# Kernel tuning notes

Measured on AMD Instinct MI355X. Metric: run time of the kernel, lower is better.

Reference implementation:

```python
import jax, jax.numpy as jnp
import numpy as np

B, S, IN, OUT = 2, 2048, 4096, 4096


def setup_inputs() -> dict:
    key = jax.random.key(0)
    k1, k2, k3, k4, k5 = jax.random.split(key, 5)
    x = jax.random.normal(k1, (B, S, IN), dtype=jnp.float32)
    weight_int8 = jax.random.randint(k2, (OUT, IN), 0, 127, dtype=jnp.int32)
    weight_scales = jax.random.uniform(k3, (OUT,), dtype=jnp.float32)
    weight_fp = jax.random.normal(k4, (OUT, IN), dtype=jnp.float32) * 0.02
    bias = jax.random.normal(k5, (OUT,), dtype=jnp.float32) * 0.02
    return {"x": x, "weight_int8": weight_int8, "weight_scales": weight_scales,
            "weight_fp": weight_fp, "bias": bias}


def reference(x, weight_int8, weight_scales, weight_fp, bias):
    # Dequantize: per-row scale / 127, cast to activation dtype (matches
    # torch: weight_int8.to(dtype) * (scales.unsqueeze(1)/127).to(dtype)).
    w_dq = weight_int8.astype(x.dtype) * (weight_scales[:, None] / 127.0).astype(x.dtype)
    # out = x @ w_dq.T + bias, over flattened leading dims
    out = jnp.einsum('bsi,oi->bso', x, w_dq) + bias
    return out
```

## Files before the change

kernel.cpp:

```cpp
#include <hip/hip_runtime.h>
#include <hip/hip_bf16.h>
#include <stdint.h>

#define MDIM 4096
#define NDIM 4096
#define KDIM 4096
#define NT   (KDIM / 64)

typedef __attribute__((ext_vector_type(4))) float  f32x4;
typedef __attribute__((ext_vector_type(4))) int    i32x4;
typedef __attribute__((ext_vector_type(8))) short  bf16x8;
typedef __attribute__((ext_vector_type(4))) float  fx4;
typedef __attribute__((ext_vector_type(4))) int    ix4;
typedef __attribute__((ext_vector_type(8))) unsigned short usx8;

__device__ static inline unsigned short f32_to_bf16_rne(float f) {
  union { float f; unsigned int u; } v; v.f = f;
  unsigned int u = v.u;
  u += 0x7fffu + ((u >> 16) & 1u);
  return (unsigned short)(u >> 16);
}

__device__ static inline void gload_lds16(const void* g, void* l) {
  __builtin_amdgcn_global_load_lds((const __attribute__((address_space(1))) void*)g,
                                   (__attribute__((address_space(3))) void*)l,
                                   16, 0, 0);
}

__device__ static inline void mfma_i8(i32x4& d, const i32x4& a, const i32x4& b) {
  asm("v_mfma_i32_16x16x64_i8 %0, %1, %2, %0" : "+v"(d) : "v"(a), "v"(b));
}


__global__ __launch_bounds__(256) void quant_both(
    const float* __restrict__ x, const int* __restrict__ w8,
    signed char* __restrict__ xq, signed char* __restrict__ wq,
    float* __restrict__ xs) {
  const int bid = blockIdx.x, t = threadIdx.x;
  if (bid < MDIM) {
    const float* row = x + (size_t)bid * KDIM + t * 16;
    fx4 v0 = *(const fx4*)(row);
    fx4 v1 = *(const fx4*)(row + 4);
    fx4 v2 = *(const fx4*)(row + 8);
    fx4 v3 = *(const fx4*)(row + 12);
    float am = 0.0f;
#pragma unroll
    for (int j = 0; j < 4; ++j) {
      am = fmaxf(am, fmaxf(__builtin_fabsf(v0[j]), __builtin_fabsf(v1[j])));
      am = fmaxf(am, fmaxf(__builtin_fabsf(v2[j]), __builtin_fabsf(v3[j])));
    }
#pragma unroll
    for (int off = 32; off; off >>= 1) am = fmaxf(am, __shfl_xor(am, off));
    __shared__ float wm[4];
    if ((t & 63) == 0) wm[t >> 6] = am;
    __syncthreads();
    am = fmaxf(fmaxf(wm[0], wm[1]), fmaxf(wm[2], wm[3]));
    am = fmaxf(am, 1e-20f);
    const float qs = 127.0f / am;
    int q[16];
#pragma unroll
    for (int j = 0; j < 4; ++j) {
      q[j]      = (int)rintf(v0[j] * qs);
      q[4 + j]  = (int)rintf(v1[j] * qs);
      q[8 + j]  = (int)rintf(v2[j] * qs);
      q[12 + j] = (int)rintf(v3[j] * qs);
    }
    i32x4 pk;
#pragma unroll
    for (int j = 0; j < 4; ++j)
      pk[j] = (q[4*j] & 255) | ((q[4*j+1] & 255) << 8) |
              ((q[4*j+2] & 255) << 16) | ((q[4*j+3] & 255) << 24);
    *(i32x4*)(xq + (size_t)bid * KDIM + t * 16) = pk;
    if (t == 0) xs[bid] = am * (1.0f / 127.0f);
  } else {
    const int n = bid - MDIM;
    const int* row = w8 + (size_t)n * KDIM + t * 16;
    ix4 w0 = *(const ix4*)(row);
    ix4 w1 = *(const ix4*)(row + 4);
    ix4 w2 = *(const ix4*)(row + 8);
    ix4 w3 = *(const ix4*)(row + 12);
    i32x4 pk;
    pk[0] = (w0[0] & 255) | ((w0[1] & 255) << 8) | ((w0[2] & 255) << 16) | ((w0[3] & 255) << 24);
    pk[1] = (w1[0] & 255) | ((w1[1] & 255) << 8) | ((w1[2] & 255) << 16) | ((w1[3] & 255) << 24);
    pk[2] = (w2[0] & 255) | ((w2[1] & 255) << 8) | ((w2[2] & 255) << 16) | ((w2[3] & 255) << 24);
    pk[3] = (w3[0] & 255) | ((w3[1] & 255) << 8) | ((w3[2] & 255) << 16) | ((w3[3] & 255) << 24);
    *(i32x4*)(wq + (size_t)n * KDIM + t * 16) = pk;
  }
}


__global__ __launch_bounds__(256, 4) void gemm_i8(
    const signed char* __restrict__ Aq,
    const signed char* __restrict__ Wq,
    const float* __restrict__ xs,
    const float* __restrict__ scales,
    const float* __restrict__ bias,
    float* __restrict__ C) {
  __shared__ signed char Ash[2 * 8192];
  __shared__ signed char Bsh[2 * 8192];

  const int tid = threadIdx.x;
  const int w   = tid >> 6;
  const int l   = tid & 63;
  const int wr  = w >> 1;
  const int wc  = w & 1;
  const int fr  = l & 15;
  const int fq  = l >> 4;

  const int id  = blockIdx.x;
  const int swz = (id & 7) * 128 + (id >> 3);
  const int bm  = swz >> 5, bn = swz & 31;

  const signed char* aorg = Aq + (size_t)(bm * 128) * KDIM;
  const signed char* borg = Wq + (size_t)(bn * 128) * KDIM;

  const int ks = (l & 3) ^ ((l >> 3) & 3);
  const size_t g_off = (size_t)(w * 16 + (l >> 2)) * KDIM + (size_t)ks * 16;
  const int    s_off = w * 1024;

#define STAGE(isB, t, P, h) do {                                                \
    const signed char* _g = ((isB) ? borg : aorg)                               \
        + (size_t)(h) * 64 * KDIM + (size_t)(t) * 64 + g_off;                   \
    signed char* _l = ((isB) ? Bsh : Ash) + ((P) + (h) * 4096 + s_off);         \
    gload_lds16(_g, _l);                                                        \
  } while (0)

  const int sl    = (fq ^ ((fr >> 1) & 3)) * 16;
  const int abase = (wr * 64 + fr) * 64 + sl;
  const int bbase = (wc * 64 + fr) * 64 + sl;

#define BAR   __builtin_amdgcn_s_barrier()
#define LGKM0 asm volatile("s_waitcnt lgkmcnt(0)" ::: "memory")
#define VM0   asm volatile("s_waitcnt vmcnt(0)" ::: "memory")

  i32x4 acc[4][4] = {};
  i32x4 a[4], b[4];

  STAGE(0, 0, 0, 0); STAGE(0, 0, 0, 1); STAGE(1, 0, 0, 0); STAGE(1, 0, 0, 1);
  VM0;
  BAR;

#pragma unroll 2
  for (int u = 0; u < NT; ++u) {
    const int cp = (u & 1) * 8192;
    const int np = cp ^ 8192;
    if (u + 1 < NT) {
      STAGE(0, u + 1, np, 0); STAGE(0, u + 1, np, 1);
      STAGE(1, u + 1, np, 0); STAGE(1, u + 1, np, 1);
    }
#pragma unroll
    for (int rb = 0; rb < 4; ++rb) a[rb] = *(const i32x4*)(Ash + cp + abase + rb * 1024);
#pragma unroll
    for (int cb = 0; cb < 4; ++cb) b[cb] = *(const i32x4*)(Bsh + cp + bbase + cb * 1024);
#pragma unroll
    for (int rb = 0; rb < 4; ++rb)
#pragma unroll
      for (int cb = 0; cb < 4; ++cb)
        mfma_i8(acc[rb][cb], a[rb], b[cb]);
    LGKM0;
    VM0;
    BAR;
  }

#undef STAGE

  const float inv127 = 1.0f / 127.0f;
  const int m_base = bm * 128 + wr * 64 + fq * 4;
  const int n_base = bn * 128 + wc * 64;
  float xr[4][4];
#pragma unroll
  for (int rb = 0; rb < 4; ++rb)
#pragma unroll
    for (int r = 0; r < 4; ++r) xr[rb][r] = xs[m_base + rb * 16 + r];
#pragma unroll
  for (int cb = 0; cb < 4; ++cb) {
    const int n = n_base + cb * 16 + fr;
    const float sw = scales[n] * inv127;
    const float bz = bias[n];
#pragma unroll
    for (int rb = 0; rb < 4; ++rb) {
      float* cp = C + (size_t)(m_base + rb * 16) * NDIM + n;
#pragma unroll
      for (int r = 0; r < 4; ++r)
        cp[(size_t)r * NDIM] = (float)acc[rb][cb][r] * (xr[rb][r] * sw) + bz;
    }
  }
}


__global__ __launch_bounds__(256) void gemm_fused(
    const float* __restrict__ X,
    const int* __restrict__ W,
    const float* __restrict__ scales,
    const float* __restrict__ bias,
    float* __restrict__ C) {
  __shared__ unsigned short As[128 * 32];
  __shared__ unsigned short Bs[128 * 32];

  const int tid = threadIdx.x;
  const int lane = tid & 63;
  const int wave = tid >> 6;
  const int wr = wave >> 1, wc = wave & 1;
  const int fr = lane & 15, fq = lane >> 4;

  int id = blockIdx.x;
  int swz = (id & 7) * 128 + (id >> 3);
  const int bm = swz >> 5, bn = swz & 31;

  const int r0 = tid >> 2;
  const int kc = (tid & 3) * 8;
  const size_t aBase = (size_t)(bm * 128 + r0) * KDIM + kc;
  const size_t bBase = (size_t)(bn * 128 + r0) * KDIM + kc;

  f32x4 acc[4][4] = {};

  for (int k0 = 0; k0 < KDIM; k0 += 32) {
    const float* xp = X + aBase + k0;
    const int*   wp = W + bBase + k0;
    fx4 x0 = *(const fx4*)xp;
    fx4 x1 = *(const fx4*)(xp + 4);
    fx4 x2 = *(const fx4*)(xp + (size_t)64 * KDIM);
    fx4 x3 = *(const fx4*)(xp + (size_t)64 * KDIM + 4);
    ix4 w0 = *(const ix4*)wp;
    ix4 w1 = *(const ix4*)(wp + 4);
    ix4 w2 = *(const ix4*)(wp + (size_t)64 * KDIM);
    ix4 w3 = *(const ix4*)(wp + (size_t)64 * KDIM + 4);

    usx8 ca, cb, cc, cd;
#pragma unroll
    for (int j = 0; j < 4; ++j) {
      ca[j] = f32_to_bf16_rne(x0[j]);  ca[j + 4] = f32_to_bf16_rne(x1[j]);
      cb[j] = f32_to_bf16_rne(x2[j]);  cb[j + 4] = f32_to_bf16_rne(x3[j]);
      cc[j] = f32_to_bf16_rne((float)w0[j]); cc[j + 4] = f32_to_bf16_rne((float)w1[j]);
      cd[j] = f32_to_bf16_rne((float)w2[j]); cd[j + 4] = f32_to_bf16_rne((float)w3[j]);
    }

    __syncthreads();
    *reinterpret_cast<usx8*>(As + tid * 8)        = ca;
    *reinterpret_cast<usx8*>(As + 2048 + tid * 8) = cb;
    *reinterpret_cast<usx8*>(Bs + tid * 8)        = cc;
    *reinterpret_cast<usx8*>(Bs + 2048 + tid * 8) = cd;
    __syncthreads();

    bf16x8 af[4], bfr[4];
    const unsigned short* ap = As + (wr * 64 + fr) * 32 + fq * 8;
    const unsigned short* bp = Bs + (wc * 64 + fr) * 32 + fq * 8;
#pragma unroll
    for (int i = 0; i < 4; ++i) {
      af[i]  = *reinterpret_cast<const bf16x8*>(ap + i * 512);
      bfr[i] = *reinterpret_cast<const bf16x8*>(bp + i * 512);
    }
#pragma unroll
    for (int im = 0; im < 4; ++im)
#pragma unroll
      for (int in_ = 0; in_ < 4; ++in_)
        acc[im][in_] = __builtin_amdgcn_mfma_f32_16x16x32_bf16(
            af[im], bfr[in_], acc[im][in_], 0, 0, 0);
  }

  const float inv127 = 1.0f / 127.0f;
#pragma unroll
  for (int in_ = 0; in_ < 4; ++in_) {
    int n = bn * 128 + wc * 64 + in_ * 16 + fr;
    float sc = scales[n] * inv127;
    float bz = bias[n];
#pragma unroll
    for (int im = 0; im < 4; ++im) {
      int m0 = bm * 128 + wr * 64 + im * 16 + fq * 4;
      float* cp = C + (size_t)m0 * NDIM + n;
#pragma unroll
      for (int r = 0; r < 4; ++r)
        cp[(size_t)r * NDIM] = acc[im][in_][r] * sc + bz;
    }
  }
}


extern "C" void kernel_launch(void* const* d_in, const int* in_sizes, int n_in,
                              void* d_out, int out_size, void* d_ws, size_t ws_size,
                              hipStream_t stream) {
  const float* x      = (const float*)d_in[0];
  const int*   w8     = (const int*)d_in[1];
  const float* scales = (const float*)d_in[2];
  const float* bias   = (const float*)d_in[4];
  float* out = (float*)d_out;

  const size_t xq_bytes = (size_t)MDIM * KDIM;
  const size_t wq_bytes = (size_t)NDIM * KDIM;
  const size_t xs_bytes = (size_t)MDIM * sizeof(float);
  const size_t need = xq_bytes + wq_bytes + xs_bytes;

  if (ws_size >= need) {
    signed char* xq = (signed char*)d_ws;
    signed char* wq = xq + xq_bytes;
    float*       xs = (float*)(wq + wq_bytes);
    quant_both<<<MDIM + NDIM, 256, 0, stream>>>(x, w8, xq, wq, xs);
    gemm_i8<<<1024, 256, 0, stream>>>(xq, wq, xs, scales, bias, out);
  } else {
    gemm_fused<<<1024, 256, 0, stream>>>(x, w8, scales, bias, out);
  }
}
```

Before: 110.2 us.

## Enlarge int8 GEMM tile to 256x128 with wave priority boost

Doubles the M dimension of each workgroup tile from 128 to 256, so each wave computes an 8x4 grid of MFMA outputs, and halves the grid to 512 blocks. A-tile LDS buffers double, occupancy hint drops to 2 blocks per CU, and setprio/sched_barrier hints wrap the MFMA section. The aim is more operand reuse per LDS load and less global traffic per output. The cost is more accumulator registers and fewer resident waves to hide latency, and with 512 blocks the load across CUs may be uneven.

```diff
diff --git a/kernel.cpp b/kernel.cpp
--- a/kernel.cpp
+++ b/kernel.cpp
@@ -89,14 +89,14 @@
 }
 
 
-__global__ __launch_bounds__(256, 4) void gemm_i8(
+__global__ __launch_bounds__(256, 2) void gemm_i8(
     const signed char* __restrict__ Aq,
     const signed char* __restrict__ Wq,
     const float* __restrict__ xs,
     const float* __restrict__ scales,
     const float* __restrict__ bias,
     float* __restrict__ C) {
-  __shared__ signed char Ash[2 * 8192];
+  __shared__ signed char Ash[2 * 16384];
   __shared__ signed char Bsh[2 * 8192];
 
   const int tid = threadIdx.x;
@@ -108,81 +108,92 @@
   const int fq  = l >> 4;
 
   const int id  = blockIdx.x;
-  const int swz = (id & 7) * 128 + (id >> 3);
-  const int bm  = swz >> 5, bn = swz & 31;
-
-  const signed char* aorg = Aq + (size_t)(bm * 128) * KDIM;
+  const int swz = (id & 7) * 64 + (id >> 3);
+  const int bm  = swz >> 5;
+  const int bn  = swz & 31;
+
+  const signed char* aorg = Aq + (size_t)(bm * 256) * KDIM;
   const signed char* borg = Wq + (size_t)(bn * 128) * KDIM;
 
   const int ks = (l & 3) ^ ((l >> 3) & 3);
   const size_t g_off = (size_t)(w * 16 + (l >> 2)) * KDIM + (size_t)ks * 16;
   const int    s_off = w * 1024;
 
-#define STAGE(isB, t, P, h) do {                                                \
-    const signed char* _g = ((isB) ? borg : aorg)                               \
-        + (size_t)(h) * 64 * KDIM + (size_t)(t) * 64 + g_off;                   \
-    signed char* _l = ((isB) ? Bsh : Ash) + ((P) + (h) * 4096 + s_off);         \
-    gload_lds16(_g, _l);                                                        \
+#define STAGE_A(t, P, h) do {                                                   \
+    const signed char* _g = aorg + (size_t)(h) * 64 * KDIM + (size_t)(t) * 64 + g_off; \
+    gload_lds16(_g, Ash + ((P) + (h) * 4096 + s_off));                          \
   } while (0)
+#define STAGE_B(t, P, h) do {                                                   \
+    const signed char* _g = borg + (size_t)(h) * 64 * KDIM + (size_t)(t) * 64 + g_off; \
+    gload_lds16(_g, Bsh + ((P) + (h) * 4096 + s_off));                          \
+  } while (0)
 
   const int sl    = (fq ^ ((fr >> 1) & 3)) * 16;
-  const int abase = (wr * 64 + fr) * 64 + sl;
-  const int bbase = (wc * 64 + fr) * 64 + sl;
-
-#define BAR   __builtin_amdgcn_s_barrier()
-#define LGKM0 asm volatile("s_waitcnt lgkmcnt(0)" ::: "memory")
-#define VM0   asm volatile("s_waitcnt vmcnt(0)" ::: "memory")
-
-  i32x4 acc[4][4] = {};
-  i32x4 a[4], b[4];
-
-  STAGE(0, 0, 0, 0); STAGE(0, 0, 0, 1); STAGE(1, 0, 0, 0); STAGE(1, 0, 0, 1);
+  const int abase = (wr * 128 + fr) * 64 + sl;
+  const int bbase = (wc * 64  + fr) * 64 + sl;
+
+#define BAR    __builtin_amdgcn_s_barrier()
+#define SCHED0 __builtin_amdgcn_sched_barrier(0)
+#define LGKM0  asm volatile("s_waitcnt lgkmcnt(0)" ::: "memory")
+#define VM0    asm volatile("s_waitcnt vmcnt(0)" ::: "memory")
+#define SP1    __builtin_amdgcn_s_setprio(1)
+#define SP0    __builtin_amdgcn_s_setprio(0)
+
+  i32x4 acc[8][4] = {};
+  i32x4 a[8], b[4];
+
+  STAGE_A(0, 0, 0); STAGE_A(0, 0, 1); STAGE_A(0, 0, 2); STAGE_A(0, 0, 3);
+  STAGE_B(0, 0, 0); STAGE_B(0, 0, 1);
   VM0;
-  BAR;
+  BAR; SCHED0;
 
 #pragma unroll 2
   for (int u = 0; u < NT; ++u) {
-    const int cp = (u & 1) * 8192;
-    const int np = cp ^ 8192;
+    const int cpa = (u & 1) * 16384, npa = cpa ^ 16384;
+    const int cpb = (u & 1) * 8192,  npb = cpb ^ 8192;
     if (u + 1 < NT) {
-      STAGE(0, u + 1, np, 0); STAGE(0, u + 1, np, 1);
-      STAGE(1, u + 1, np, 0); STAGE(1, u + 1, np, 1);
-    }
-#pragma unroll
-    for (int rb = 0; rb < 4; ++rb) a[rb] = *(const i32x4*)(Ash + cp + abase + rb * 1024);
-#pragma unroll
-    for (int cb = 0; cb < 4; ++cb) b[cb] = *(const i32x4*)(Bsh + cp + bbase + cb * 1024);
-#pragma unroll
-    for (int rb = 0; rb < 4; ++rb)
-#pragma unroll
-      for (int cb = 0; cb < 4; ++cb)
-        mfma_i8(acc[rb][cb], a[rb], b[cb]);
+      STAGE_A(u + 1, npa, 0); STAGE_A(u + 1, npa, 1);
+      STAGE_A(u + 1, npa, 2); STAGE_A(u + 1, npa, 3);
+      STAGE_B(u + 1, npb, 0); STAGE_B(u + 1, npb, 1);
+    }
+#pragma unroll
+    for (int rb = 0; rb < 8; ++rb) a[rb] = *(const i32x4*)(Ash + cpa + abase + rb * 1024);
+#pragma unroll
+    for (int nc = 0; nc < 4; ++nc) b[nc] = *(const i32x4*)(Bsh + cpb + bbase + nc * 1024);
+    SP1;
+#pragma unroll
+    for (int rb = 0; rb < 8; ++rb)
+#pragma unroll
+      for (int nc = 0; nc < 4; ++nc)
+        mfma_i8(acc[rb][nc], a[rb], b[nc]);
+    SP0;
     LGKM0;
     VM0;
-    BAR;
-  }
-
-#undef STAGE
+    BAR; SCHED0;
+  }
+
+#undef STAGE_A
+#undef STAGE_B
 
   const float inv127 = 1.0f / 127.0f;
-  const int m_base = bm * 128 + wr * 64 + fq * 4;
+  const int m_base = bm * 256 + wr * 128 + fq * 4;
   const int n_base = bn * 128 + wc * 64;
-  float xr[4][4];
-#pragma unroll
-  for (int rb = 0; rb < 4; ++rb)
+  float xr[8][4];
+#pragma unroll
+  for (int rb = 0; rb < 8; ++rb)
 #pragma unroll
     for (int r = 0; r < 4; ++r) xr[rb][r] = xs[m_base + rb * 16 + r];
 #pragma unroll
-  for (int cb = 0; cb < 4; ++cb) {
-    const int n = n_base + cb * 16 + fr;
+  for (int nc = 0; nc < 4; ++nc) {
+    const int n = n_base + nc * 16 + fr;
     const float sw = scales[n] * inv127;
     const float bz = bias[n];
 #pragma unroll
-    for (int rb = 0; rb < 4; ++rb) {
+    for (int rb = 0; rb < 8; ++rb) {
       float* cp = C + (size_t)(m_base + rb * 16) * NDIM + n;
 #pragma unroll
       for (int r = 0; r < 4; ++r)
-        cp[(size_t)r * NDIM] = (float)acc[rb][cb][r] * (xr[rb][r] * sw) + bz;
+        cp[(size_t)r * NDIM] = (float)acc[rb][nc][r] * (xr[rb][r] * sw) + bz;
     }
   }
 }
@@ -295,7 +306,7 @@
     signed char* wq = xq + xq_bytes;
     float*       xs = (float*)(wq + wq_bytes);
     quant_both<<<MDIM + NDIM, 256, 0, stream>>>(x, w8, xq, wq, xs);
-    gemm_i8<<<1024, 256, 0, stream>>>(xq, wq, xs, scales, bias, out);
+    gemm_i8<<<512, 256, 0, stream>>>(xq, wq, xs, scales, bias, out);
   } else {
     gemm_fused<<<1024, 256, 0, stream>>>(x, w8, scales, bias, out);
   }
```

New measurement: 106.0 us. -3.8%, faster.
